# Kernel tuning notes

Hardware: AMD Instinct MI355X
Metric: run time of the kernel (lower is better)

Reference implementation:

```python
import jax, jax.numpy as jnp
import numpy as np

B, S, D, H, E = 4, 2048, 512, 8, 4  # batch, seq, embed, heads, expand
HD = D // H


def setup_inputs() -> dict:
    key = jax.random.key(0)
    ks = jax.random.split(key, 9)
    s = lambda k, shape, fan: jax.random.normal(k, shape, jnp.float32) * (fan ** -0.5)
    return {
        "x": jax.random.normal(ks[0], (B, S, D), jnp.float32),
        "Wq": s(ks[1], (D, D), D),
        "Wk": s(ks[2], (D, D), D),
        "Wv": s(ks[3], (D, D), D),
        "Wo": s(ks[4], (D, D), D),
        "W1": s(ks[5], (D, D * E), D),
        "b1": jnp.zeros((D * E,), jnp.float32),
        "W2": s(ks[6], (D * E, D), D * E),
        "b2": jnp.zeros((D,), jnp.float32),
    }


def _encoder_layer(x, Wq, Wk, Wv, Wo, W1, b1, W2, b2):
    # NOTE: source computes InstanceNorm1d twice but discards both results -> no-ops.
    scale = D ** -0.25  # applied to BOTH q and k (net 1/sqrt(embed_dim))
    q = (x @ Wq).reshape(B, S, H, HD).transpose(0, 2, 1, 3) * scale  # [B,H,S,hd]
    k = (x @ Wk).reshape(B, S, H, HD).transpose(0, 2, 1, 3) * scale
    v = (x @ Wv).reshape(B, S, H, HD).transpose(0, 2, 1, 3)
    scores = jnp.einsum('bhqd,bhkd->bhqk', q, k)  # [B,H,S,S]
    attn = jax.nn.softmax(scores, axis=-1)
    o = jnp.einsum('bhqk,bhkd->bhqd', attn, v)  # [B,H,S,hd]
    o = o.transpose(0, 2, 1, 3).reshape(B, S, D)
    x = o @ Wo + x  # residual 1
    h = jax.nn.gelu(x @ W1 + b1, approximate=True)  # torch GELU(approximate='tanh')
    return h @ W2 + b2 + x  # residual 2 (dropout=0, eval)


def reference(x, Wq, Wk, Wv, Wo, W1, b1, W2, b2):
    return _encoder_layer(x, Wq, Wk, Wv, Wo, W1, b1, W2, b2)
```

## Files before the change

### kernel.cpp

```cpp
#include <hip/hip_runtime.h>
#include <hip/hip_bf16.h>


typedef __bf16 bf16;
typedef __attribute__((ext_vector_type(8))) __bf16 bf16x8;
typedef __attribute__((ext_vector_type(4))) __bf16 bf16x4;
typedef __attribute__((ext_vector_type(4))) float f32x4;
typedef __attribute__((ext_vector_type(16))) float f32x16;
typedef __attribute__((ext_vector_type(4))) short s16x4;
typedef __attribute__((ext_vector_type(2))) unsigned int u32x2;
typedef __attribute__((ext_vector_type(4))) unsigned int u32x4;

#define LOG2E 1.4426950408889634f
#define SCORE_SCALE 0.044194173824159216f
#define SCALE_L2E (SCORE_SCALE * LOG2E)
#define FIXED_M 12.0f

#if __has_builtin(__builtin_amdgcn_exp2f)
#define EXP2(x) __builtin_amdgcn_exp2f(x)
#else
#define EXP2(x) exp2f(x)
#endif

__device__ __forceinline__ void gl_lds16(const bf16* g, bf16* l) {
  __builtin_amdgcn_global_load_lds(
      (const __attribute__((address_space(1))) unsigned int*)g,
      (__attribute__((address_space(3))) unsigned int*)l, 16, 0, 0);
}

__device__ __forceinline__ float gelu_tanh(float x) {
  float u = 0.7978845608028654f * (x + 0.044715f * x * x * x);
  float e = EXP2(u * (2.0f * LOG2E));
  float th = 1.0f - 2.0f / (e + 1.0f);
  return 0.5f * x * (1.0f + th);
}

__device__ __forceinline__ f32x4 mfma_bf16(bf16x8 a, bf16x8 b, f32x4 c) {
  return __builtin_amdgcn_mfma_f32_16x16x32_bf16(a, b, c, 0, 0, 0);
}
__device__ __forceinline__ f32x16 mfma32x16(bf16x8 a, bf16x8 b, f32x16 c) {
  return __builtin_amdgcn_mfma_f32_32x32x16_bf16(a, b, c, 0, 0, 0);
}

__device__ __forceinline__ void plswap(unsigned int& a, unsigned int& b) {
  asm volatile("v_permlane32_swap_b32 %0, %1" : "+v"(a), "+v"(b));
}

template <int MODE, typename OutT, int TN>
__global__ __launch_bounds__(256, 2) void gemm_bt(
    const bf16* __restrict__ A, const bf16* __restrict__ Bt,
    OutT* __restrict__ C, const float* __restrict__ bias,
    const float* __restrict__ resf, const bf16* __restrict__ resb,
    int M, int N, int K) {
  constexpr int MI = (TN == 128) ? 4 : 2;
  __shared__ __align__(16) bf16 sA[2][128 * 32];
  __shared__ __align__(16) bf16 sB[2][TN * 32];
  const int tid = threadIdx.x;
  const int lane = tid & 63;
  const int quad = lane >> 4, lc = lane & 15;
  const int wave = tid >> 6;
  const int wr = (TN == 128) ? (wave >> 1) : wave;
  const int wc = (TN == 128) ? (wave & 1) : 0;
  const int m0 = blockIdx.y * 128, n0 = blockIdx.x * TN;

  const int srow = tid >> 2;
  const int kc = (tid & 3) * 8;
  const bf16* Ag1 = A + (size_t)(m0 + srow) * K + kc;
  const bf16* Ag2 = A + (size_t)(m0 + 64 + srow) * K + kc;
  const bf16* Bg1 = Bt + (size_t)(n0 + srow) * K + kc;
  const bf16* Bg2 = Bt + (size_t)(n0 + 64 + srow) * K + kc;
  const int o1 = tid * 8, o2 = (tid + 256) * 8;

  f32x4 acc[MI][4];
#pragma unroll
  for (int mi = 0; mi < MI; ++mi)
#pragma unroll
    for (int ni = 0; ni < 4; ++ni) acc[mi][ni] = (f32x4){0.f, 0.f, 0.f, 0.f};

  gl_lds16(Ag1, sA[0] + o1);
  gl_lds16(Ag2, sA[0] + o2);
  gl_lds16(Bg1, sB[0] + o1);
  if (TN == 128) gl_lds16(Bg2, sB[0] + o2);
  Ag1 += 32; Ag2 += 32; Bg1 += 32; Bg2 += 32;

  const int kIters = K >> 5;
  for (int kt = 0; kt < kIters; ++kt) {
    __syncthreads();
    const bf16* cA = sA[kt & 1];
    const bf16* cB = sB[kt & 1];
    if (kt + 1 < kIters) {
      bf16* nA = sA[(kt + 1) & 1];
      bf16* nB = sB[(kt + 1) & 1];
      gl_lds16(Ag1, nA + o1);
      gl_lds16(Ag2, nA + o2);
      gl_lds16(Bg1, nB + o1);
      if (TN == 128) gl_lds16(Bg2, nB + o2);
      Ag1 += 32; Ag2 += 32; Bg1 += 32; Bg2 += 32;
    }

    bf16x8 af[MI], bfm[4];
#pragma unroll
    for (int i = 0; i < MI; ++i)
      af[i] =
          *(const bf16x8*)(cA + ((wr * (16 * MI) + i * 16 + lc) * 32 + quad * 8));
#pragma unroll
    for (int i = 0; i < 4; ++i)
      bfm[i] = *(const bf16x8*)(cB + ((wc * 64 + i * 16 + lc) * 32 + quad * 8));
#pragma unroll
    for (int mi = 0; mi < MI; ++mi)
#pragma unroll
      for (int ni = 0; ni < 4; ++ni)
        acc[mi][ni] = mfma_bf16(af[mi], bfm[ni], acc[mi][ni]);
  }

#pragma unroll
  for (int mi = 0; mi < MI; ++mi) {
#pragma unroll
    for (int r = 0; r < 4; ++r) {
      const int row = m0 + wr * (16 * MI) + mi * 16 + quad * 4 + r;
#pragma unroll
      for (int ni = 0; ni < 4; ++ni) {
        const int col = n0 + wc * 64 + ni * 16 + lc;
        const size_t idx = (size_t)row * N + col;
        float v = acc[mi][ni][r];
        if (MODE == 1) v += resf[idx];
        if (MODE == 2) v = gelu_tanh(v + bias[col]);
        if (MODE == 3) v += bias[col] + (float)resb[idx];
        C[idx] = (OutT)v;
      }
    }
  }
}

__global__ __launch_bounds__(256, 2) void flash_attn(
    const bf16* __restrict__ QKV, const bf16* __restrict__ Vt,
    bf16* __restrict__ O) {
  const int tid = threadIdx.x;
  const int lane = tid & 63, wave = tid >> 6;
  const int lo5 = lane & 31, hi = lane >> 5;
  const int bh = blockIdx.y, b = bh >> 3, h = bh & 7;
  const int q0 = blockIdx.x * 128 + wave * 32;

  __shared__ __align__(16) bf16 sK[3][4096];
  __shared__ __align__(16) bf16 sV[3][4096];

  const bf16* Qrow = QKV + (size_t)(b * 2048 + q0 + lo5) * 1536 + h * 64;
  bf16x8 qf[4];
#pragma unroll
  for (int i = 0; i < 4; ++i) qf[i] = *(const bf16x8*)(Qrow + i * 16 + hi * 8);

  const int colsw = (((lane & 7) ^ (lane >> 3)) << 3);
  const bf16* Kg0 = QKV + (size_t)b * 2048 * 1536 + 512 + (size_t)h * 64 +
                    (size_t)(wave * 16 + (lane >> 3)) * 1536 + colsw;
  const bf16* Vg0 = Vt + (size_t)bh * 64 * 2048 +
                    (size_t)(wave * 16 + (lane >> 3)) * 2048 + colsw;
  const int stag = wave * 1024;
  const int m7 = lo5 & 7;

  f32x16 oacc[2];
  oacc[0] = (f32x16)(0.f);
  oacc[1] = (f32x16)(0.f);
  float rsum = 0.f;

  auto stage = [&](int buf, int t) {
    gl_lds16(Kg0 + (size_t)t * 64 * 1536, sK[buf] + stag);
    gl_lds16(Kg0 + (size_t)(t * 64 + 8) * 1536, sK[buf] + stag + 512);
    gl_lds16(Vg0 + t * 64, sV[buf] + stag);
    gl_lds16(Vg0 + t * 64 + 8 * 2048, sV[buf] + stag + 512);
  };
  stage(0, 0);
  stage(1, 1);

  for (int kt = 0; kt < 32; ++kt) {
    if (kt == 31)
      asm volatile("s_waitcnt vmcnt(0)\ns_barrier" ::: "memory");
    else
      asm volatile("s_waitcnt vmcnt(4)\ns_barrier" ::: "memory");
    const int cb = kt % 3;
    const bf16* cK = sK[cb];
    const bf16* cV = sV[cb];
    if (kt + 2 < 32) stage((kt + 2) % 3, kt + 2);

    bf16x8 paw[4];
#pragma unroll
    for (int hl = 0; hl < 2; ++hl) {
      f32x16 st = (f32x16)(0.f);
      const int R = hl * 32 + lo5;
      __builtin_amdgcn_s_setprio(1);
#pragma unroll
      for (int i = 0; i < 4; ++i) {
        bf16x8 kf =
            *(const bf16x8*)(cK + R * 64 + (((2 * i + hi) ^ m7) << 3));
        st = mfma32x16(kf, qf[i], st);
      }
      __builtin_amdgcn_s_setprio(0);
      unsigned int q32[4][2];
#pragma unroll
      for (int g = 0; g < 4; ++g) {
        bf16x4 pb;
#pragma unroll
        for (int j = 0; j < 4; ++j) {
          float p = EXP2(st[4 * g + j] * SCALE_L2E - FIXED_M);
          rsum += p;
          pb[j] = (bf16)p;
        }
        u32x2 w2 = __builtin_bit_cast(u32x2, pb);
        q32[g][0] = w2[0];
        q32[g][1] = w2[1];
      }
#pragma unroll
      for (int t = 0; t < 2; ++t) {
        unsigned int a0 = q32[2 * t][0], a1 = q32[2 * t][1];
        unsigned int b0 = q32[2 * t + 1][0], b1 = q32[2 * t + 1][1];
        plswap(a0, b0);
        plswap(a1, b1);
        u32x4 f = {a0, a1, b0, b1};
        paw[hl * 2 + t] = __builtin_bit_cast(bf16x8, f);
      }
    }

    __builtin_amdgcn_s_setprio(1);
#pragma unroll
    for (int dh = 0; dh < 2; ++dh) {
      const int Rd = dh * 32 + lo5;
#pragma unroll
      for (int w = 0; w < 4; ++w) {
        bf16x8 vf =
            *(const bf16x8*)(cV + Rd * 64 + (((2 * w + hi) ^ m7) << 3));
        oacc[dh] = mfma32x16(paw[w], vf, oacc[dh]);
      }
    }
    __builtin_amdgcn_s_setprio(0);
  }

  rsum += __shfl_xor(rsum, 32, 64);
  const size_t obase = (size_t)(b * 2048 + q0) * 512 + h * 64;
#pragma unroll
  for (int r = 0; r < 16; ++r) {
    const int qloc = (r & 3) + 8 * (r >> 2) + 4 * hi;
    const float inv = 1.0f / __shfl(rsum, qloc, 64);
#pragma unroll
    for (int dh = 0; dh < 2; ++dh)
      O[obase + (size_t)qloc * 512 + dh * 32 + lo5] =
          (bf16)(oacc[dh][r] * inv);
  }
}

__global__ __launch_bounds__(256) void prep(
    const float* __restrict__ x, const float* __restrict__ Wq,
    const float* __restrict__ Wk, const float* __restrict__ Wv,
    const float* __restrict__ Wo, const float* __restrict__ W1,
    const float* __restrict__ W2, bf16* __restrict__ xb,
    bf16* __restrict__ WqkvT, bf16* __restrict__ WoT, bf16* __restrict__ W1T,
    bf16* __restrict__ W2T) {
  const int bid = blockIdx.x;
  if (bid < 4096) {
    const size_t i = ((size_t)bid * 256 + threadIdx.x) * 4;
    const float4 v = *(const float4*)(x + i);
    bf16x4 o;
    o[0] = (bf16)v.x; o[1] = (bf16)v.y; o[2] = (bf16)v.z; o[3] = (bf16)v.w;
    *(bf16x4*)(xb + i) = o;
    return;
  }
  const int t = bid - 4096;
  const float* in;
  bf16* out;
  int in_ld, out_ld, bx, by;
  if (t < 1024) {
    const int q = t >> 8, r = t & 255;
    bx = r & 15; by = r >> 4; in_ld = 512; out_ld = 512;
    in = (q == 0) ? Wq : (q == 1) ? Wk : (q == 2) ? Wv : Wo;
    out = (q == 0) ? WqkvT
          : (q == 1) ? WqkvT + 512 * 512
          : (q == 2) ? WqkvT + 2 * 512 * 512
                     : WoT;
  } else if (t < 2048) {
    const int r = t - 1024;
    bx = r & 63; by = r >> 6; in_ld = 2048; out_ld = 512;
    in = W1; out = W1T;
  } else {
    const int r = t - 2048;
    bx = r & 15; by = r >> 4; in_ld = 512; out_ld = 2048;
    in = W2; out = W2T;
  }
  __shared__ __align__(16) bf16 tl[32][33];
  const int tx = threadIdx.x & 31, ty = threadIdx.x >> 5;
  const int n0 = bx * 32, k0 = by * 32;
#pragma unroll
  for (int i = 0; i < 4; ++i)
    tl[ty + 8 * i][tx] = (bf16)in[(size_t)(k0 + ty + 8 * i) * in_ld + n0 + tx];
  __syncthreads();
#pragma unroll
  for (int i = 0; i < 4; ++i)
    out[(size_t)(n0 + ty + 8 * i) * out_ld + k0 + tx] = tl[tx][ty + 8 * i];
}

__global__ __launch_bounds__(256) void transpose_v(
    const bf16* __restrict__ QKV, bf16* __restrict__ Vt) {
  __shared__ __align__(16) bf16 t[32][33];
  const int tx = threadIdx.x & 31, ty = threadIdx.x >> 5;
  const int bh = blockIdx.z, b = bh >> 3, h = bh & 7;
  const bf16* ip = QKV + (size_t)b * 2048 * 1536 + 1024 + h * 64;
  bf16* op = Vt + (size_t)bh * 64 * 2048;
  const int d0 = blockIdx.x * 32, s0 = blockIdx.y * 32;
#pragma unroll
  for (int i = 0; i < 4; ++i)
    t[ty + 8 * i][tx] = ip[(size_t)(s0 + ty + 8 * i) * 1536 + d0 + tx];
  __syncthreads();
#pragma unroll
  for (int i = 0; i < 4; ++i)
    op[(size_t)(d0 + ty + 8 * i) * 2048 + s0 + tx] = t[tx][ty + 8 * i];
}

extern "C" void kernel_launch(void* const* d_in, const int* in_sizes, int n_in,
                              void* d_out, int out_size, void* d_ws,
                              size_t ws_size, hipStream_t stream) {
  const float* x = (const float*)d_in[0];
  const float* Wq = (const float*)d_in[1];
  const float* Wk = (const float*)d_in[2];
  const float* Wv = (const float*)d_in[3];
  const float* Wo = (const float*)d_in[4];
  const float* W1 = (const float*)d_in[5];
  const float* b1 = (const float*)d_in[6];
  const float* W2 = (const float*)d_in[7];
  const float* b2 = (const float*)d_in[8];
  float* out = (float*)d_out;

  char* ws = (char*)d_ws;
  size_t off = 0;
  auto alloc = [&](size_t bytes) {
    char* p = ws + off;
    off += (bytes + 255) & ~(size_t)255;
    return p;
  };
  bf16* WqkvT = (bf16*)alloc(1536ULL * 512 * 2);
  bf16* WoT = (bf16*)alloc(512ULL * 512 * 2);
  bf16* W1T = (bf16*)alloc(2048ULL * 512 * 2);
  bf16* W2T = (bf16*)alloc(512ULL * 2048 * 2);
  bf16* xb = (bf16*)alloc(8192ULL * 512 * 2);
  bf16* QKV = (bf16*)alloc(8192ULL * 1536 * 2);
  bf16* Vt = (bf16*)alloc(32ULL * 64 * 2048 * 2);
  bf16* attn = (bf16*)alloc(8192ULL * 512 * 2);
  bf16* x2 = xb;
  bf16* hbuf = QKV;

  const dim3 tb(256);
  prep<<<dim3(7168), tb, 0, stream>>>(x, Wq, Wk, Wv, Wo, W1, W2, xb, WqkvT,
                                      WoT, W1T, W2T);
  gemm_bt<0, bf16, 128><<<dim3(12, 64), tb, 0, stream>>>(
      xb, WqkvT, QKV, nullptr, nullptr, nullptr, 8192, 1536, 512);
  transpose_v<<<dim3(2, 64, 32), tb, 0, stream>>>(QKV, Vt);
  flash_attn<<<dim3(16, 32), tb, 0, stream>>>(QKV, Vt, attn);
  gemm_bt<1, bf16, 64><<<dim3(8, 64), tb, 0, stream>>>(
      attn, WoT, x2, nullptr, x, nullptr, 8192, 512, 512);
  gemm_bt<2, bf16, 128><<<dim3(16, 64), tb, 0, stream>>>(
      x2, W1T, hbuf, b1, nullptr, nullptr, 8192, 2048, 512);
  gemm_bt<3, float, 64><<<dim3(8, 64), tb, 0, stream>>>(
      hbuf, W2T, out, b2, nullptr, x2, 8192, 512, 2048);
}
```

Before: 256.6 us.

## Software-pipeline PV with next QK tile, remap blocks per XCD

Restructures the flash attention loop so the PV MFMAs of the previous tile are issued together with the QK and softmax of the current tile. This needs a fourth V LDS buffer so V stays resident one iteration longer. It also remaps block indices so each XCD handles a contiguous set of batch-heads, aiming for better L2 reuse of K and V. The QK accumulation is split into two independent accumulators to shorten the MFMA dependency chain. The extra LDS raises shared memory use, which may affect the two-blocks-per-CU occupancy.

```diff
diff --git a/kernel.cpp b/kernel.cpp
--- a/kernel.cpp
+++ b/kernel.cpp
@@ -138,11 +138,15 @@
   const int tid = threadIdx.x;
   const int lane = tid & 63, wave = tid >> 6;
   const int lo5 = lane & 31, hi = lane >> 5;
-  const int bh = blockIdx.y, b = bh >> 3, h = bh & 7;
-  const int q0 = blockIdx.x * 128 + wave * 32;
+  const int lin = blockIdx.y * 16 + blockIdx.x;
+  const int xcd = lin & 7, slot = lin >> 3;
+  const int bh = xcd * 4 + (slot >> 4);
+  const int qt = slot & 15;
+  const int b = bh >> 3, h = bh & 7;
+  const int q0 = qt * 128 + wave * 32;
 
   __shared__ __align__(16) bf16 sK[3][4096];
-  __shared__ __align__(16) bf16 sV[3][4096];
+  __shared__ __align__(16) bf16 sV[4][4096];
 
   const bf16* Qrow = QKV + (size_t)(b * 2048 + q0 + lo5) * 1536 + h * 64;
   bf16x8 qf[4];
@@ -162,38 +166,33 @@
   oacc[1] = (f32x16)(0.f);
   float rsum = 0.f;
 
-  auto stage = [&](int buf, int t) {
-    gl_lds16(Kg0 + (size_t)t * 64 * 1536, sK[buf] + stag);
-    gl_lds16(Kg0 + (size_t)(t * 64 + 8) * 1536, sK[buf] + stag + 512);
-    gl_lds16(Vg0 + t * 64, sV[buf] + stag);
-    gl_lds16(Vg0 + t * 64 + 8 * 2048, sV[buf] + stag + 512);
+  auto stage = [&](int t) {
+    bf16* dk = sK[t % 3] + stag;
+    bf16* dv = sV[t & 3] + stag;
+    gl_lds16(Kg0 + (size_t)t * 64 * 1536, dk);
+    gl_lds16(Kg0 + (size_t)(t * 64 + 8) * 1536, dk + 512);
+    gl_lds16(Vg0 + t * 64, dv);
+    gl_lds16(Vg0 + t * 64 + 8 * 2048, dv + 512);
   };
-  stage(0, 0);
-  stage(1, 1);
-
-  for (int kt = 0; kt < 32; ++kt) {
-    if (kt == 31)
-      asm volatile("s_waitcnt vmcnt(0)\ns_barrier" ::: "memory");
-    else
-      asm volatile("s_waitcnt vmcnt(4)\ns_barrier" ::: "memory");
-    const int cb = kt % 3;
-    const bf16* cK = sK[cb];
-    const bf16* cV = sV[cb];
-    if (kt + 2 < 32) stage((kt + 2) % 3, kt + 2);
-
-    bf16x8 paw[4];
+
+  bf16x8 paw[4];
+
+  auto qk_softmax = [&](const bf16* cK) {
 #pragma unroll
     for (int hl = 0; hl < 2; ++hl) {
-      f32x16 st = (f32x16)(0.f);
       const int R = hl * 32 + lo5;
+      bf16x8 kf0 = *(const bf16x8*)(cK + R * 64 + (((0 + hi) ^ m7) << 3));
+      bf16x8 kf1 = *(const bf16x8*)(cK + R * 64 + (((2 + hi) ^ m7) << 3));
+      bf16x8 kf2 = *(const bf16x8*)(cK + R * 64 + (((4 + hi) ^ m7) << 3));
+      bf16x8 kf3 = *(const bf16x8*)(cK + R * 64 + (((6 + hi) ^ m7) << 3));
+      f32x16 st0 = (f32x16)(0.f), st1 = (f32x16)(0.f);
       __builtin_amdgcn_s_setprio(1);
-#pragma unroll
-      for (int i = 0; i < 4; ++i) {
-        bf16x8 kf =
-            *(const bf16x8*)(cK + R * 64 + (((2 * i + hi) ^ m7) << 3));
-        st = mfma32x16(kf, qf[i], st);
-      }
+      st0 = mfma32x16(kf0, qf[0], st0);
+      st1 = mfma32x16(kf1, qf[1], st1);
+      st0 = mfma32x16(kf2, qf[2], st0);
+      st1 = mfma32x16(kf3, qf[3], st1);
       __builtin_amdgcn_s_setprio(0);
+      f32x16 st = st0 + st1;
       unsigned int q32[4][2];
 #pragma unroll
       for (int g = 0; g < 4; ++g) {
@@ -218,7 +217,9 @@
         paw[hl * 2 + t] = __builtin_bit_cast(bf16x8, f);
       }
     }
-
+  };
+
+  auto pv = [&](const bf16* cV) {
     __builtin_amdgcn_s_setprio(1);
 #pragma unroll
     for (int dh = 0; dh < 2; ++dh) {
@@ -231,7 +232,26 @@
       }
     }
     __builtin_amdgcn_s_setprio(0);
-  }
+  };
+
+  stage(0);
+  stage(1);
+  asm volatile("s_waitcnt vmcnt(4)\ns_barrier" ::: "memory");
+  stage(2);
+  qk_softmax(sK[0]);
+
+  for (int kt = 1; kt < 32; ++kt) {
+    if (kt == 31)
+      asm volatile("s_waitcnt vmcnt(0)\ns_barrier" ::: "memory");
+    else
+      asm volatile("s_waitcnt vmcnt(4)\ns_barrier" ::: "memory");
+    if (kt + 2 < 32) stage(kt + 2);
+    const bf16* cK = sK[kt % 3];
+    const bf16* cVp = sV[(kt + 3) & 3];
+    pv(cVp);
+    qk_softmax(cK);
+  }
+  pv(sV[31 & 3]);
 
   rsum += __shfl_xor(rsum, 32, 64);
   const size_t obase = (size_t)(b * 2048 + q0) * 512 + h * 64;
```

After: 257.5 us. About the same (+0.4%).
